# Kernel optimization log

Hardware: AMD Instinct MI355X
Metric: run time of the kernel (lower is better)

The kernel has to match this reference:

```python
import jax, jax.numpy as jnp
import numpy as np


def setup_inputs() -> dict:
    key = jax.random.key(0)
    B, N = 32, 262144
    z = jax.random.uniform(key, (B, N, 3), dtype=jnp.float32)
    return {"z": z}


def reference(z):
    # order == 'xyz': lexicographic sort of the N points by (x, y, z),
    # x most significant. jnp.lexsort treats the LAST key as primary,
    # so pass (z_key, y_key, x_key). Sorts along axis=-1 (points),
    # batched over B for free.
    keys = (z[:, :, 2], z[:, :, 1], z[:, :, 0])  # each [B, N]
    idx_pa = jnp.lexsort(keys, axis=-1)          # [B, N] permutation: sorted -> original
    # Original computes torch.sort(gather(arange, idx_pa))[1], which is the
    # inverse permutation of idx_pa; argsort of a permutation inverts it.
    idx_re = jnp.argsort(idx_pa, axis=-1)        # [B, N] original -> sorted position
    return idx_pa, idx_re
```

## Files before the change

### kernel.cpp

```cpp
#include <hip/hip_runtime.h>
#include <stdint.h>

typedef unsigned int u32;
typedef unsigned long long u64;
typedef unsigned char u8;

#define BROWS 32
#define NPTS  262144
#define LOG_NPTS 18
#define CB 256
#define RCAP 1280
#define ROWSTRIDE_FIX (CB * RCAP)
#define CCAP 1536
#define FB2 1024

#define MCH 8192
#define MWG 1024
#define TCH 8192
#define TWG 1024

__device__ __forceinline__ u32 g18_of(float z0) {
    int b = (int)(z0 * 262144.0f);
    return (u32)(b < 0 ? 0 : (b > 262143 ? 262143 : b));
}

__global__ __launch_bounds__(256) void hist_kernel(const float* __restrict__ z,
                                                   u32* __restrict__ counts) {
    __shared__ u32 h[CB];
    for (int i = threadIdx.x; i < CB; i += 256) h[i] = 0;
    __syncthreads();
    int r = blockIdx.x >> 6;
    int c = blockIdx.x & 63;
    size_t base = ((size_t)r << LOG_NPTS) + (size_t)c * 4096;
    for (int k = 0; k < 16; ++k) {
        float z0 = z[(base + (size_t)(k * 256 + threadIdx.x)) * 3];
        atomicAdd(&h[g18_of(z0) >> 10], 1u);
    }
    __syncthreads();
    for (int i = threadIdx.x; i < CB; i += 256)
        if (h[i]) atomicAdd(&counts[r * CB + i], h[i]);
}

__global__ __launch_bounds__(256) void scan_dense(const u32* __restrict__ counts,
                                                  u32* __restrict__ offsets,
                                                  u32* __restrict__ gcur) {
    int r = blockIdx.x, t = threadIdx.x;
    __shared__ u32 sc[CB];
    u32 v = counts[r * CB + t];
    sc[t] = v;
    __syncthreads();
    u32 own = v;
    for (int off = 1; off < CB; off <<= 1) {
        u32 a = (t >= off) ? sc[t - off] : 0;
        __syncthreads();
        sc[t] += a;
        __syncthreads();
    }
    u32 ex = sc[t] - own;
    offsets[r * CB + t] = ex;
    gcur[r * CB + t] = ex;
}

__global__ __launch_bounds__(256) void scan_fixed(const u32* __restrict__ gcur,
                                                  u32* __restrict__ offsets,
                                                  u32* __restrict__ counts) {
    int r = blockIdx.x, t = threadIdx.x;
    __shared__ u32 sc[CB];
    u32 cnt = gcur[r * CB + t];
    if (cnt > RCAP) cnt = RCAP;
    counts[r * CB + t] = cnt;
    sc[t] = cnt;
    __syncthreads();
    u32 own = cnt;
    for (int off = 1; off < CB; off <<= 1) {
        u32 a = (t >= off) ? sc[t - off] : 0;
        __syncthreads();
        sc[t] += a;
        __syncthreads();
    }
    offsets[r * CB + t] = sc[t] - own;
}

__global__ __launch_bounds__(MWG) void ms_scatter(const float* __restrict__ z,
                                                  u32* __restrict__ gcur,
                                                  u64* __restrict__ rec,
                                                  int fixedMode) {
    __shared__ u32 h[CB], sc[CB], gb[CB], wtot[4];
    __shared__ u64 reord[MCH];
    int t = threadIdx.x;
    int r = blockIdx.x >> 5;
    int c = blockIdx.x & 31;
    if (t < CB) h[t] = 0;
    __syncthreads();

    u32 base_pt = (u32)(c * MCH + t * 8);
    const float4* zf4 = (const float4*)(z + ((size_t)r << LOG_NPTS) * 3 + (size_t)base_pt * 3);
    float4 f[6];
#pragma unroll
    for (int j = 0; j < 6; ++j) f[j] = zf4[j];
    const float* ff = (const float*)f;

    u32 mpk[8];
    u64 mv[8];
#pragma unroll
    for (int k = 0; k < 8; ++k) {
        float f0 = ff[3 * k];
        u32 k0 = __float_as_uint(f0);
        u32 g = g18_of(f0);
        u32 b = g >> 10;
        mv[k] = ((u64)k0 << 32) | ((g & 1023u) << 18) | (base_pt + (u32)k);
        u32 arr = atomicAdd(&h[b], 1u);
        mpk[k] = (b << 16) | arr;
    }
    __syncthreads();
    u32 scan_s = 0, scan_v = 0;
    int lane = t & 63, wv = t >> 6;
    if (t < CB) {
        scan_v = h[t];
        scan_s = scan_v;
        for (int off = 1; off < 64; off <<= 1) {
            u32 o = __shfl_up(scan_s, off, 64);
            if (lane >= off) scan_s += o;
        }
        if (lane == 63) wtot[wv] = scan_s;
    }
    __syncthreads();
    if (t < CB) {
        u32 wb = 0;
        if (wv > 0) wb += wtot[0];
        if (wv > 1) wb += wtot[1];
        if (wv > 2) wb += wtot[2];
        sc[t] = wb + scan_s - scan_v;
        gb[t] = atomicAdd(&gcur[r * CB + t], h[t]);
    }
    __syncthreads();
#pragma unroll
    for (int k = 0; k < 8; ++k) {
        u32 b = mpk[k] >> 16, arr = mpk[k] & 0xFFFFu;
        reord[sc[b] + arr] = mv[k];
    }
    __syncthreads();
    size_t rowrec = fixedMode ? (size_t)r * ROWSTRIDE_FIX : ((size_t)r << LOG_NPTS);
#pragma unroll
    for (int k = 0; k < 8; ++k) {
        u32 s = (u32)(k * MWG + t);
        u64 v = reord[s];
        u32 b = g18_of(__uint_as_float((u32)(v >> 32))) >> 10;
        u32 local = gb[b] + (s - sc[b]);
        if (fixedMode) {
            if (local < (u32)RCAP)
                rec[rowrec + (size_t)b * RCAP + local] = v;
        } else {
            rec[rowrec + local] = v;
        }
    }
}

__global__ __launch_bounds__(256) void fine_sort(const u64* __restrict__ rec,
                                                 const float* __restrict__ z,
                                                 const u32* __restrict__ offsets,
                                                 const u32* __restrict__ counts,
                                                 int* __restrict__ out_pa,
                                                 int fixedMode) {
    __shared__ u64 kv[CCAP];
    __shared__ u32 fh[FB2], fex[FB2], wtot[4];
    int t = threadIdx.x;
    int g = blockIdx.x;
    int r = g >> 8;
    int cbk = g & 255;
    size_t rowrec = fixedMode ? (size_t)r * ROWSTRIDE_FIX : ((size_t)r << LOG_NPTS);
    u32 rdstart = fixedMode ? (u32)cbk * RCAP : offsets[g];
    u32 wrstart = offsets[g];
    u32 count = counts[g];
    u32 cap = fixedMode ? (u32)RCAP : (u32)CCAP;
    if (count > cap) count = cap;
    for (int i = t; i < FB2; i += 256) fh[i] = 0;
    __syncthreads();

    u32 rid[6], rk0[6], rpk[6];
#pragma unroll
    for (int k = 0; k < 6; ++k) {
        u32 s = (u32)t + (u32)k * 256u;
        rpk[k] = 0xFFFFFFFFu;
        if (s < count) {
            u64 v = rec[rowrec + rdstart + s];
            u32 tag = (u32)v;
            u32 fb = (tag >> 18) & 1023u;
            rid[k] = tag & 0x3FFFFu;
            rk0[k] = (u32)(v >> 32);
            u32 arr = atomicAdd(&fh[fb], 1u);
            rpk[k] = (fb << 16) | arr;
        }
    }
    __syncthreads();
    {
        u32 v0 = fh[4 * t], v1 = fh[4 * t + 1], v2 = fh[4 * t + 2], v3 = fh[4 * t + 3];
        u32 tsum = v0 + v1 + v2 + v3;
        u32 s = tsum;
        int lane = t & 63, w = t >> 6;
        for (int off = 1; off < 64; off <<= 1) {
            u32 o = __shfl_up(s, off, 64);
            if (lane >= off) s += o;
        }
        if (lane == 63) wtot[w] = s;
        __syncthreads();
        u32 wbase = 0;
        if (w > 0) wbase += wtot[0];
        if (w > 1) wbase += wtot[1];
        if (w > 2) wbase += wtot[2];
        u32 ex = wbase + s - tsum;
        fex[4 * t] = ex;
        fex[4 * t + 1] = ex + v0;
        fex[4 * t + 2] = ex + v0 + v1;
        fex[4 * t + 3] = ex + v0 + v1 + v2;
    }
    __syncthreads();
#pragma unroll
    for (int k = 0; k < 6; ++k) {
        if (rpk[k] != 0xFFFFFFFFu) {
            u32 fb = rpk[k] >> 16, arr = rpk[k] & 0xFFFFu;
            if (fh[fb] > 1)
                kv[fex[fb] + arr] = ((u64)rk0[k] << 32) | rid[k];
        }
    }
    __syncthreads();

    size_t orow = (size_t)r << LOG_NPTS;
    size_t zrow = ((size_t)r << LOG_NPTS) * 3;
#pragma unroll
    for (int k = 0; k < 6; ++k) {
        if (rpk[k] == 0xFFFFFFFFu) continue;
        u32 fb = rpk[k] >> 16;
        u32 cnt = fh[fb];
        u32 base = fex[fb];
        u32 pos = base;
        if (cnt > 1) {
            u32 rank = 0;
            u32 a0 = rk0[k], ai = rid[k];
            u32 a1 = 0, a2 = 0;
            bool aLoaded = false;
            for (u32 j = 0; j < cnt; ++j) {
                u64 bv = kv[base + j];
                u32 b0 = (u32)(bv >> 32);
                if (b0 < a0) { ++rank; continue; }
                if (b0 == a0) {
                    u32 bi = (u32)bv & 0x3FFFFu;
                    if (bi == ai) continue;
                    if (!aLoaded) {
                        a1 = __float_as_uint(z[zrow + (size_t)ai * 3 + 1]);
                        a2 = __float_as_uint(z[zrow + (size_t)ai * 3 + 2]);
                        aLoaded = true;
                    }
                    u32 b1 = __float_as_uint(z[zrow + (size_t)bi * 3 + 1]);
                    if (b1 < a1) { ++rank; continue; }
                    if (b1 == a1) {
                        u32 b2 = __float_as_uint(z[zrow + (size_t)bi * 3 + 2]);
                        rank += (b2 < a2) || (b2 == a2 && bi < ai);
                    }
                }
            }
            pos = base + rank;
        }
        out_pa[orow + wrstart + pos] = (int)rid[k];
    }
}

__global__ __launch_bounds__(TWG) void trans_ms(const int* __restrict__ out_pa,
                                                u32* __restrict__ tcur,
                                                u32* __restrict__ pairs) {
    __shared__ u32 h[CB], sc[CB], gb[CB], wtot[4];
    __shared__ u32 reord[TCH];
    __shared__ u8 rb8[TCH];
    int t = threadIdx.x;
    int r = blockIdx.x >> 5;
    int c = blockIdx.x & 31;
    if (t < CB) h[t] = 0;
    __syncthreads();
    u32 mpk[8], mv[8];
#pragma unroll
    for (int k = 0; k < 8; ++k) {
        u32 p = (u32)(c * TCH + k * TWG + t);
        u32 si = (u32)out_pa[((size_t)r << LOG_NPTS) + p];
        u32 b = si >> 10;
        mv[k] = ((si & 1023u) << 18) | p;
        u32 arr = atomicAdd(&h[b], 1u);
        mpk[k] = (b << 16) | arr;
    }
    __syncthreads();
    u32 scan_s = 0, scan_v = 0;
    int lane = t & 63, wv = t >> 6;
    if (t < CB) {
        scan_v = h[t];
        scan_s = scan_v;
        for (int off = 1; off < 64; off <<= 1) {
            u32 o = __shfl_up(scan_s, off, 64);
            if (lane >= off) scan_s += o;
        }
        if (lane == 63) wtot[wv] = scan_s;
    }
    __syncthreads();
    if (t < CB) {
        u32 wbase = 0;
        if (wv > 0) wbase += wtot[0];
        if (wv > 1) wbase += wtot[1];
        if (wv > 2) wbase += wtot[2];
        sc[t] = wbase + scan_s - scan_v;
        gb[t] = atomicAdd(&tcur[r * CB + t], h[t]);
    }
    __syncthreads();
#pragma unroll
    for (int k = 0; k < 8; ++k) {
        u32 b = mpk[k] >> 16, arr = mpk[k] & 0xFFFFu;
        u32 p = sc[b] + arr;
        reord[p] = mv[k];
        rb8[p] = (u8)b;
    }
    __syncthreads();
#pragma unroll
    for (int k = 0; k < 8; ++k) {
        u32 s = (u32)(k * TWG + t);
        u32 v = reord[s];
        u32 b = rb8[s];
        u32 local = s - sc[b];
        pairs[((size_t)r << LOG_NPTS) + (size_t)b * 1024 + gb[b] + local] = v;
    }
}

__global__ __launch_bounds__(256) void trans_write(const u32* __restrict__ pairs,
                                                   int* __restrict__ out_re) {
    __shared__ u32 buf[1024];
    int g = blockIdx.x;
    int r = g >> 8, b = g & 255;
    size_t base = ((size_t)r << LOG_NPTS) + (size_t)b * 1024;
#pragma unroll
    for (int k = 0; k < 4; ++k) {
        u32 v = pairs[base + (size_t)(k * 256 + threadIdx.x)];
        buf[v >> 18] = v & 0x3FFFFu;
    }
    __syncthreads();
#pragma unroll
    for (int k = 0; k < 4; ++k) {
        int j = k * 256 + threadIdx.x;
        out_re[base + (size_t)j] = (int)buf[j];
    }
}

extern "C" void kernel_launch(void* const* d_in, const int* in_sizes, int n_in,
                              void* d_out, int out_size, void* d_ws, size_t ws_size,
                              hipStream_t stream) {
    const float* z = (const float*)d_in[0];
    int* out_pa = (int*)d_out;
    int* out_re = out_pa + (size_t)BROWS * NPTS;

    char* ws = (char*)d_ws;
    u32* counts  = (u32*)(ws);
    u32* offsets = (u32*)(ws + (64u << 10));
    u32* gcur    = (u32*)(ws + (128u << 10));
    u32* tcur    = (u32*)(ws + (160u << 10));
    u64* rec     = (u64*)(ws + (1u << 20));
    u32* pairs   = (u32*)(ws + (1u << 20) + (80ull << 20));

    size_t need = (1ull << 20) + (80ull << 20) + (32ull << 20);
    int fixedMode = (ws_size >= need) ? 1 : 0;

    if (fixedMode) {
        hipMemsetAsync(gcur, 0, 2 * (size_t)BROWS * CB * sizeof(u32), stream);
        ms_scatter<<<BROWS * 32, MWG, 0, stream>>>(z, gcur, rec, 1);
        scan_fixed<<<BROWS, 256, 0, stream>>>(gcur, offsets, counts);
        fine_sort<<<BROWS * CB, 256, 0, stream>>>(rec, z, offsets, counts, out_pa, 1);
    } else {
        hipMemsetAsync(counts, 0, (size_t)BROWS * CB * sizeof(u32), stream);
        hipMemsetAsync(tcur, 0, (size_t)BROWS * CB * sizeof(u32), stream);
        hist_kernel<<<BROWS * 64, 256, 0, stream>>>(z, counts);
        scan_dense<<<BROWS, 256, 0, stream>>>(counts, offsets, gcur);
        ms_scatter<<<BROWS * 32, MWG, 0, stream>>>(z, gcur, rec, 0);
        fine_sort<<<BROWS * CB, 256, 0, stream>>>(rec, z, offsets, counts, out_pa, 0);
    }
    trans_ms<<<BROWS * 32, TWG, 0, stream>>>(out_pa, tcur, pairs);
    trans_write<<<BROWS * CB, 256, 0, stream>>>(pairs, out_re);
}
```

Before: 134.4 us.

## Fuse fixed-mode bucket scan into fine_sort and widen fine_sort workgroups

Removes the separate scan_fixed launch by having each fine_sort block recompute its row's 256-bucket exclusive prefix scan with wave shuffles. The tcur memset is replaced by each block zeroing its own tcur entry, which trims the fixed-mode memset to cover only gcur. fine_sort now runs 512 threads with 3 records per thread instead of 256 threads with 6, so the 1024-bin histogram scan handles 2 bins per thread. This saves launches and a dependent kernel boundary, at the cost of 256 blocks per row each redundantly redoing the row scan and higher register/LDS pressure per block.

```diff
diff --git a/kernel.cpp b/kernel.cpp
--- a/kernel.cpp
+++ b/kernel.cpp
@@ -16,6 +16,8 @@
 
 #define MCH 8192
 #define MWG 1024
+#define FWG 512
+#define FRT 3
 #define TCH 8192
 #define TWG 1024
 
@@ -59,26 +61,6 @@
     u32 ex = sc[t] - own;
     offsets[r * CB + t] = ex;
     gcur[r * CB + t] = ex;
-}
-
-__global__ __launch_bounds__(256) void scan_fixed(const u32* __restrict__ gcur,
-                                                  u32* __restrict__ offsets,
-                                                  u32* __restrict__ counts) {
-    int r = blockIdx.x, t = threadIdx.x;
-    __shared__ u32 sc[CB];
-    u32 cnt = gcur[r * CB + t];
-    if (cnt > RCAP) cnt = RCAP;
-    counts[r * CB + t] = cnt;
-    sc[t] = cnt;
-    __syncthreads();
-    u32 own = cnt;
-    for (int off = 1; off < CB; off <<= 1) {
-        u32 a = (t >= off) ? sc[t - off] : 0;
-        __syncthreads();
-        sc[t] += a;
-        __syncthreads();
-    }
-    offsets[r * CB + t] = sc[t] - own;
 }
 
 __global__ __launch_bounds__(MWG) void ms_scatter(const float* __restrict__ z,
@@ -156,31 +138,67 @@
     }
 }
 
-__global__ __launch_bounds__(256) void fine_sort(const u64* __restrict__ rec,
+__global__ __launch_bounds__(FWG) void fine_sort(const u64* __restrict__ rec,
                                                  const float* __restrict__ z,
+                                                 const u32* __restrict__ gcur,
                                                  const u32* __restrict__ offsets,
                                                  const u32* __restrict__ counts,
+                                                 u32* __restrict__ tcur,
                                                  int* __restrict__ out_pa,
                                                  int fixedMode) {
     __shared__ u64 kv[CCAP];
-    __shared__ u32 fh[FB2], fex[FB2], wtot[4];
+    __shared__ u32 fh[FB2], fex[FB2], wtot[8];
+    __shared__ u32 scx[CB];
     int t = threadIdx.x;
     int g = blockIdx.x;
-    int r = g >> 8;
-    int cbk = g & 255;
-    size_t rowrec = fixedMode ? (size_t)r * ROWSTRIDE_FIX : ((size_t)r << LOG_NPTS);
-    u32 rdstart = fixedMode ? (u32)cbk * RCAP : offsets[g];
-    u32 wrstart = offsets[g];
-    u32 count = counts[g];
-    u32 cap = fixedMode ? (u32)RCAP : (u32)CCAP;
-    if (count > cap) count = cap;
-    for (int i = t; i < FB2; i += 256) fh[i] = 0;
-    __syncthreads();
-
-    u32 rid[6], rk0[6], rpk[6];
-#pragma unroll
-    for (int k = 0; k < 6; ++k) {
-        u32 s = (u32)t + (u32)k * 256u;
+    int r = g >> 8, cbk = g & 255;
+    if (t == 0) tcur[g] = 0;
+
+    u32 count, wrstart, rdstart;
+    size_t rowrec;
+    int lane = t & 63;
+    if (fixedMode) {
+        u32 sv = 0, ss = 0;
+        int wv4 = t >> 6;
+        if (t < CB) {
+            u32 cc = gcur[r * CB + t];
+            if (cc > RCAP) cc = RCAP;
+            sv = cc; ss = cc;
+            for (int off = 1; off < 64; off <<= 1) {
+                u32 o = __shfl_up(ss, off, 64);
+                if (lane >= off) ss += o;
+            }
+            if (lane == 63) wtot[wv4] = ss;
+        }
+        for (int i = t; i < FB2; i += FWG) fh[i] = 0;
+        __syncthreads();
+        if (t < CB) {
+            u32 wb = 0;
+            if (wv4 > 0) wb += wtot[0];
+            if (wv4 > 1) wb += wtot[1];
+            if (wv4 > 2) wb += wtot[2];
+            scx[t] = wb + ss - sv;
+        }
+        __syncthreads();
+        wrstart = scx[cbk];
+        u32 cc = gcur[r * CB + cbk];
+        count = cc > RCAP ? RCAP : cc;
+        rowrec = (size_t)r * ROWSTRIDE_FIX;
+        rdstart = (u32)cbk * RCAP;
+    } else {
+        for (int i = t; i < FB2; i += FWG) fh[i] = 0;
+        __syncthreads();
+        wrstart = offsets[g];
+        count = counts[g];
+        if (count > CCAP) count = CCAP;
+        rowrec = (size_t)r << LOG_NPTS;
+        rdstart = offsets[g];
+    }
+
+    u32 rid[FRT], rk0[FRT], rpk[FRT];
+#pragma unroll
+    for (int k = 0; k < FRT; ++k) {
+        u32 s = (u32)t + (u32)(k * FWG);
         rpk[k] = 0xFFFFFFFFu;
         if (s < count) {
             u64 v = rec[rowrec + rdstart + s];
@@ -194,10 +212,10 @@
     }
     __syncthreads();
     {
-        u32 v0 = fh[4 * t], v1 = fh[4 * t + 1], v2 = fh[4 * t + 2], v3 = fh[4 * t + 3];
-        u32 tsum = v0 + v1 + v2 + v3;
+        u32 v0 = fh[2 * t], v1 = fh[2 * t + 1];
+        u32 tsum = v0 + v1;
         u32 s = tsum;
-        int lane = t & 63, w = t >> 6;
+        int w = t >> 6;
         for (int off = 1; off < 64; off <<= 1) {
             u32 o = __shfl_up(s, off, 64);
             if (lane >= off) s += o;
@@ -205,18 +223,15 @@
         if (lane == 63) wtot[w] = s;
         __syncthreads();
         u32 wbase = 0;
-        if (w > 0) wbase += wtot[0];
-        if (w > 1) wbase += wtot[1];
-        if (w > 2) wbase += wtot[2];
+#pragma unroll
+        for (int w2 = 0; w2 < 7; ++w2) if (w > w2) wbase += wtot[w2];
         u32 ex = wbase + s - tsum;
-        fex[4 * t] = ex;
-        fex[4 * t + 1] = ex + v0;
-        fex[4 * t + 2] = ex + v0 + v1;
-        fex[4 * t + 3] = ex + v0 + v1 + v2;
-    }
-    __syncthreads();
-#pragma unroll
-    for (int k = 0; k < 6; ++k) {
+        fex[2 * t] = ex;
+        fex[2 * t + 1] = ex + v0;
+    }
+    __syncthreads();
+#pragma unroll
+    for (int k = 0; k < FRT; ++k) {
         if (rpk[k] != 0xFFFFFFFFu) {
             u32 fb = rpk[k] >> 16, arr = rpk[k] & 0xFFFFu;
             if (fh[fb] > 1)
@@ -228,7 +243,7 @@
     size_t orow = (size_t)r << LOG_NPTS;
     size_t zrow = ((size_t)r << LOG_NPTS) * 3;
 #pragma unroll
-    for (int k = 0; k < 6; ++k) {
+    for (int k = 0; k < FRT; ++k) {
         if (rpk[k] == 0xFFFFFFFFu) continue;
         u32 fb = rpk[k] >> 16;
         u32 cnt = fh[fb];
@@ -364,17 +379,17 @@
     int fixedMode = (ws_size >= need) ? 1 : 0;
 
     if (fixedMode) {
-        hipMemsetAsync(gcur, 0, 2 * (size_t)BROWS * CB * sizeof(u32), stream);
+        hipMemsetAsync(gcur, 0, (size_t)BROWS * CB * sizeof(u32), stream);
         ms_scatter<<<BROWS * 32, MWG, 0, stream>>>(z, gcur, rec, 1);
-        scan_fixed<<<BROWS, 256, 0, stream>>>(gcur, offsets, counts);
-        fine_sort<<<BROWS * CB, 256, 0, stream>>>(rec, z, offsets, counts, out_pa, 1);
+        fine_sort<<<BROWS * CB, FWG, 0, stream>>>(rec, z, gcur, offsets, counts,
+                                                  tcur, out_pa, 1);
     } else {
         hipMemsetAsync(counts, 0, (size_t)BROWS * CB * sizeof(u32), stream);
-        hipMemsetAsync(tcur, 0, (size_t)BROWS * CB * sizeof(u32), stream);
         hist_kernel<<<BROWS * 64, 256, 0, stream>>>(z, counts);
         scan_dense<<<BROWS, 256, 0, stream>>>(counts, offsets, gcur);
         ms_scatter<<<BROWS * 32, MWG, 0, stream>>>(z, gcur, rec, 0);
-        fine_sort<<<BROWS * CB, 256, 0, stream>>>(rec, z, offsets, counts, out_pa, 0);
+        fine_sort<<<BROWS * CB, FWG, 0, stream>>>(rec, z, gcur, offsets, counts,
+                                                  tcur, out_pa, 0);
     }
     trans_ms<<<BROWS * 32, TWG, 0, stream>>>(out_pa, tcur, pairs);
     trans_write<<<BROWS * CB, 256, 0, stream>>>(pairs, out_re);
```

After: 136.7 us. Within noise of the previous version (+1.7%).

## Pack sort records into 32 bits with 22-bit x-prefix and refine via gathers

Applied to the files above, without the earlier changes.

Shrinks the intermediate records from 64-bit (full x key plus tag) to 32-bit by packing 4 extra x-quantization bits, the 10-bit fine bucket and the 18-bit point index. This halves the scatter/read traffic and LDS footprint in ms_scatter and fine_sort. Ties on the 22-bit prefix now fall back to gathering x, y, z from global memory. The bucket id is kept in a byte array instead of being recomputed. The tcur memset is folded into fine_sort, whose blocks zero tcur themselves.

```diff
diff --git a/kernel.cpp b/kernel.cpp
--- a/kernel.cpp
+++ b/kernel.cpp
@@ -19,9 +19,9 @@
 #define TCH 8192
 #define TWG 1024
 
-__device__ __forceinline__ u32 g18_of(float z0) {
-    int b = (int)(z0 * 262144.0f);
-    return (u32)(b < 0 ? 0 : (b > 262143 ? 262143 : b));
+__device__ __forceinline__ u32 g22_of(float z0) {
+    int b = (int)(z0 * 4194304.0f);
+    return (u32)(b < 0 ? 0 : (b > 4194303 ? 4194303 : b));
 }
 
 __global__ __launch_bounds__(256) void hist_kernel(const float* __restrict__ z,
@@ -34,7 +34,7 @@
     size_t base = ((size_t)r << LOG_NPTS) + (size_t)c * 4096;
     for (int k = 0; k < 16; ++k) {
         float z0 = z[(base + (size_t)(k * 256 + threadIdx.x)) * 3];
-        atomicAdd(&h[g18_of(z0) >> 10], 1u);
+        atomicAdd(&h[g22_of(z0) >> 14], 1u);
     }
     __syncthreads();
     for (int i = threadIdx.x; i < CB; i += 256)
@@ -83,10 +83,11 @@
 
 __global__ __launch_bounds__(MWG) void ms_scatter(const float* __restrict__ z,
                                                   u32* __restrict__ gcur,
-                                                  u64* __restrict__ rec,
+                                                  u32* __restrict__ rec,
                                                   int fixedMode) {
     __shared__ u32 h[CB], sc[CB], gb[CB], wtot[4];
-    __shared__ u64 reord[MCH];
+    __shared__ u32 reord[MCH];
+    __shared__ u8 rb8[MCH];
     int t = threadIdx.x;
     int r = blockIdx.x >> 5;
     int c = blockIdx.x & 31;
@@ -100,15 +101,12 @@
     for (int j = 0; j < 6; ++j) f[j] = zf4[j];
     const float* ff = (const float*)f;
 
-    u32 mpk[8];
-    u64 mv[8];
-#pragma unroll
-    for (int k = 0; k < 8; ++k) {
-        float f0 = ff[3 * k];
-        u32 k0 = __float_as_uint(f0);
-        u32 g = g18_of(f0);
-        u32 b = g >> 10;
-        mv[k] = ((u64)k0 << 32) | ((g & 1023u) << 18) | (base_pt + (u32)k);
+    u32 mpk[8], mv[8];
+#pragma unroll
+    for (int k = 0; k < 8; ++k) {
+        u32 g = g22_of(ff[3 * k]);
+        u32 b = g >> 14;
+        mv[k] = ((g & 15u) << 28) | (((g >> 4) & 1023u) << 18) | (base_pt + (u32)k);
         u32 arr = atomicAdd(&h[b], 1u);
         mpk[k] = (b << 16) | arr;
     }
@@ -137,15 +135,17 @@
 #pragma unroll
     for (int k = 0; k < 8; ++k) {
         u32 b = mpk[k] >> 16, arr = mpk[k] & 0xFFFFu;
-        reord[sc[b] + arr] = mv[k];
+        u32 p = sc[b] + arr;
+        reord[p] = mv[k];
+        rb8[p] = (u8)b;
     }
     __syncthreads();
     size_t rowrec = fixedMode ? (size_t)r * ROWSTRIDE_FIX : ((size_t)r << LOG_NPTS);
 #pragma unroll
     for (int k = 0; k < 8; ++k) {
         u32 s = (u32)(k * MWG + t);
-        u64 v = reord[s];
-        u32 b = g18_of(__uint_as_float((u32)(v >> 32))) >> 10;
+        u32 v = reord[s];
+        u32 b = rb8[s];
         u32 local = gb[b] + (s - sc[b]);
         if (fixedMode) {
             if (local < (u32)RCAP)
@@ -156,18 +156,19 @@
     }
 }
 
-__global__ __launch_bounds__(256) void fine_sort(const u64* __restrict__ rec,
+__global__ __launch_bounds__(256) void fine_sort(const u32* __restrict__ rec,
                                                  const float* __restrict__ z,
                                                  const u32* __restrict__ offsets,
                                                  const u32* __restrict__ counts,
+                                                 u32* __restrict__ tcur,
                                                  int* __restrict__ out_pa,
                                                  int fixedMode) {
-    __shared__ u64 kv[CCAP];
+    __shared__ u32 kv[CCAP];
     __shared__ u32 fh[FB2], fex[FB2], wtot[4];
     int t = threadIdx.x;
     int g = blockIdx.x;
-    int r = g >> 8;
-    int cbk = g & 255;
+    int r = g >> 8, cbk = g & 255;
+    if (t == 0) tcur[g] = 0;
     size_t rowrec = fixedMode ? (size_t)r * ROWSTRIDE_FIX : ((size_t)r << LOG_NPTS);
     u32 rdstart = fixedMode ? (u32)cbk * RCAP : offsets[g];
     u32 wrstart = offsets[g];
@@ -177,17 +178,16 @@
     for (int i = t; i < FB2; i += 256) fh[i] = 0;
     __syncthreads();
 
-    u32 rid[6], rk0[6], rpk[6];
+    u32 rid[6], rres[6], rpk[6];
 #pragma unroll
     for (int k = 0; k < 6; ++k) {
         u32 s = (u32)t + (u32)k * 256u;
         rpk[k] = 0xFFFFFFFFu;
         if (s < count) {
-            u64 v = rec[rowrec + rdstart + s];
-            u32 tag = (u32)v;
+            u32 tag = rec[rowrec + rdstart + s];
             u32 fb = (tag >> 18) & 1023u;
             rid[k] = tag & 0x3FFFFu;
-            rk0[k] = (u32)(v >> 32);
+            rres[k] = tag >> 28;
             u32 arr = atomicAdd(&fh[fb], 1u);
             rpk[k] = (fb << 16) | arr;
         }
@@ -220,7 +220,7 @@
         if (rpk[k] != 0xFFFFFFFFu) {
             u32 fb = rpk[k] >> 16, arr = rpk[k] & 0xFFFFu;
             if (fh[fb] > 1)
-                kv[fex[fb] + arr] = ((u64)rk0[k] << 32) | rid[k];
+                kv[fex[fb] + arr] = (rres[k] << 18) | rid[k];
         }
     }
     __syncthreads();
@@ -236,27 +236,30 @@
         u32 pos = base;
         if (cnt > 1) {
             u32 rank = 0;
-            u32 a0 = rk0[k], ai = rid[k];
-            u32 a1 = 0, a2 = 0;
+            u32 ares = rres[k], ai = rid[k];
+            u32 a0 = 0, a1 = 0, a2 = 0;
             bool aLoaded = false;
             for (u32 j = 0; j < cnt; ++j) {
-                u64 bv = kv[base + j];
-                u32 b0 = (u32)(bv >> 32);
-                if (b0 < a0) { ++rank; continue; }
-                if (b0 == a0) {
-                    u32 bi = (u32)bv & 0x3FFFFu;
+                u32 bv = kv[base + j];
+                u32 bres = bv >> 18;
+                if (bres < ares) { ++rank; continue; }
+                if (bres == ares) {
+                    u32 bi = bv & 0x3FFFFu;
                     if (bi == ai) continue;
                     if (!aLoaded) {
+                        a0 = __float_as_uint(z[zrow + (size_t)ai * 3]);
                         a1 = __float_as_uint(z[zrow + (size_t)ai * 3 + 1]);
                         a2 = __float_as_uint(z[zrow + (size_t)ai * 3 + 2]);
                         aLoaded = true;
                     }
+                    u32 b0 = __float_as_uint(z[zrow + (size_t)bi * 3]);
+                    if (b0 < a0) { ++rank; continue; }
+                    if (b0 > a0) continue;
                     u32 b1 = __float_as_uint(z[zrow + (size_t)bi * 3 + 1]);
                     if (b1 < a1) { ++rank; continue; }
-                    if (b1 == a1) {
-                        u32 b2 = __float_as_uint(z[zrow + (size_t)bi * 3 + 2]);
-                        rank += (b2 < a2) || (b2 == a2 && bi < ai);
-                    }
+                    if (b1 > a1) continue;
+                    u32 b2 = __float_as_uint(z[zrow + (size_t)bi * 3 + 2]);
+                    rank += (b2 < a2) || (b2 == a2 && bi < ai);
                 }
             }
             pos = base + rank;
@@ -357,24 +360,25 @@
     u32* offsets = (u32*)(ws + (64u << 10));
     u32* gcur    = (u32*)(ws + (128u << 10));
     u32* tcur    = (u32*)(ws + (160u << 10));
-    u64* rec     = (u64*)(ws + (1u << 20));
-    u32* pairs   = (u32*)(ws + (1u << 20) + (80ull << 20));
-
-    size_t need = (1ull << 20) + (80ull << 20) + (32ull << 20);
+    u32* rec     = (u32*)(ws + (1u << 20));
+    u32* pairs   = (u32*)(ws + (1u << 20) + (48ull << 20));
+
+    size_t need = (1ull << 20) + (48ull << 20) + (32ull << 20);
     int fixedMode = (ws_size >= need) ? 1 : 0;
 
     if (fixedMode) {
-        hipMemsetAsync(gcur, 0, 2 * (size_t)BROWS * CB * sizeof(u32), stream);
+        hipMemsetAsync(gcur, 0, (size_t)BROWS * CB * sizeof(u32), stream);
         ms_scatter<<<BROWS * 32, MWG, 0, stream>>>(z, gcur, rec, 1);
         scan_fixed<<<BROWS, 256, 0, stream>>>(gcur, offsets, counts);
-        fine_sort<<<BROWS * CB, 256, 0, stream>>>(rec, z, offsets, counts, out_pa, 1);
+        fine_sort<<<BROWS * CB, 256, 0, stream>>>(rec, z, offsets, counts,
+                                                  tcur, out_pa, 1);
     } else {
         hipMemsetAsync(counts, 0, (size_t)BROWS * CB * sizeof(u32), stream);
-        hipMemsetAsync(tcur, 0, (size_t)BROWS * CB * sizeof(u32), stream);
         hist_kernel<<<BROWS * 64, 256, 0, stream>>>(z, counts);
         scan_dense<<<BROWS, 256, 0, stream>>>(counts, offsets, gcur);
         ms_scatter<<<BROWS * 32, MWG, 0, stream>>>(z, gcur, rec, 0);
-        fine_sort<<<BROWS * CB, 256, 0, stream>>>(rec, z, offsets, counts, out_pa, 0);
+        fine_sort<<<BROWS * CB, 256, 0, stream>>>(rec, z, offsets, counts,
+                                                  tcur, out_pa, 0);
     }
     trans_ms<<<BROWS * 32, TWG, 0, stream>>>(out_pa, tcur, pairs);
     trans_write<<<BROWS * CB, 256, 0, stream>>>(pairs, out_re);
```

Measured after the change: 132.3 us (median of 2 runs). No clear change (-1.6%).
